# Performance work log

Measured on AMD Instinct MI355X. Metric: run time of the kernel, lower is better.

## Reference

```python
import jax, jax.numpy as jnp
import numpy as np

B, D, H, DH, DFF = 2, 1024, 16, 64, 4096
NB, NR, S = 24, 8, 512
SCALE_DEPTH = 1.4
FSQ_DIM, FSQ_LEVELS = 32, 8
EPS = 1e-5


def rmsnorm(x, w):
    var = jnp.mean(x * x, axis=-1, keepdims=True)
    return x * jax.lax.rsqrt(var + EPS) * w


def rope_cos_sin(position):
    # position: [B] int -> cos/sin [B, DH/2]
    inv = 1.0 / (10000.0 ** (jnp.arange(0, DH, 2, dtype=jnp.float32) / DH))
    ang = position.astype(jnp.float32)[:, None] * inv[None, :]
    return jnp.cos(ang), jnp.sin(ang)


def apply_rope(x, cos, sin):
    # x: [B, H, 1, DH]
    x1, x2 = jnp.split(x, 2, axis=-1)
    c = cos[:, None, None, :]
    s = sin[:, None, None, :]
    return jnp.concatenate([x1 * c - x2 * s, x1 * s + x2 * c], axis=-1)


def run_lm(hidden, cache_k, cache_v, params, cos, sin, n_layers):
    # hidden [B,1,D]; cache_k/v [L,B,H,S,DH]; params: stacked per-layer weights.
    scale = SCALE_DEPTH / np.sqrt(n_layers)  # MuP residual scale
    inv_sqrt_dh = 1.0 / np.sqrt(DH)

    def body(h, xs):
        ln1, wq, wk, wv, wo, ln2, wg, wu, wd, ck, cv = xs
        res = h
        hn = rmsnorm(h, ln1)
        q = (hn @ wq).reshape(B, 1, H, DH).transpose(0, 2, 1, 3)
        k = (hn @ wk).reshape(B, 1, H, DH).transpose(0, 2, 1, 3)
        v = (hn @ wv).reshape(B, 1, H, DH).transpose(0, 2, 1, 3)
        q = apply_rope(q, cos, sin)
        k = apply_rope(k, cos, sin)
        nk = jnp.concatenate([ck, k], axis=2)  # [B,H,S+1,DH]
        nv = jnp.concatenate([cv, v], axis=2)
        att = jnp.einsum('bhqd,bhkd->bhqk', q, nk) * inv_sqrt_dh
        p = jax.nn.softmax(att, axis=-1)
        o = jnp.einsum('bhqk,bhkd->bhqd', p, nv).transpose(0, 2, 1, 3).reshape(B, 1, D) @ wo
        h = res + o * scale
        res = h
        hn = rmsnorm(h, ln2)
        mlp = (jax.nn.silu(hn @ wg) * (hn @ wu)) @ wd
        h = res + mlp * scale
        return h, (nk, nv)

    ln1, wq, wk, wv, wo, ln2, wg, wu, wd = params
    hidden, (nk, nv) = jax.lax.scan(
        body, hidden, (ln1, wq, wk, wv, wo, ln2, wg, wu, wd, cache_k, cache_v))
    return hidden, nk, nv


def fsq(x, w_in, w_out):
    # finite scalar quantization with straight-through rounding
    z = jnp.tanh(x @ w_in)
    half = (FSQ_LEVELS - 1) / 2.0
    zq = jnp.round(z * half) / half
    zq = z + jax.lax.stop_gradient(zq - z)
    return zq @ w_out


def _forward(position, embed, base_k, base_v, res_k, res_v,
             base_ln1, base_ln2, base_wq, base_wk, base_wv, base_wo,
             base_wg, base_wu, base_wd, base_norm,
             res_ln1, res_ln2, res_wq, res_wk, res_wv, res_wo,
             res_wg, res_wu, res_wd, res_norm,
             fsq_in, fsq_out, stop_proj_w, stop_proj_b, stop_head_w, stop_head_b):
    cos, sin = rope_cos_sin(position)
    hidden, bnk, bnv = run_lm(
        embed, base_k, base_v,
        (base_ln1, base_wq, base_wk, base_wv, base_wo, base_ln2, base_wg, base_wu, base_wd),
        cos, sin, NB)
    lm_hidden = rmsnorm(hidden, base_norm)
    lm_fsq = fsq(lm_hidden, fsq_in, fsq_out)
    stop_logit = jax.nn.silu(lm_hidden @ stop_proj_w + stop_proj_b) @ stop_head_w + stop_head_b
    res_in = lm_fsq + embed
    rh, rnk, rnv = run_lm(
        res_in, res_k, res_v,
        (res_ln1, res_wq, res_wk, res_wv, res_wo, res_ln2, res_wg, res_wu, res_wd),
        cos, sin, NR)
    rh = rmsnorm(rh, res_norm)
    return (lm_fsq, rh, stop_logit, bnk, bnv, rnk, rnv)


def setup_inputs() -> dict:
    key = jax.random.key(0)
    ks = iter(jax.random.split(key, 40))

    def p(shape, scale=0.02):
        return jax.random.normal(next(ks), shape, dtype=jnp.float32) * scale

    return {
        'embed': jax.random.normal(next(ks), (B, 1, D), jnp.float32),
        'position': jax.random.randint(next(ks), (B,), 0, S),
        'base_k': jax.random.normal(next(ks), (NB, B, H, S, DH), jnp.float32),
        'base_v': jax.random.normal(next(ks), (NB, B, H, S, DH), jnp.float32),
        'res_k': jax.random.normal(next(ks), (NR, B, H, S, DH), jnp.float32),
        'res_v': jax.random.normal(next(ks), (NR, B, H, S, DH), jnp.float32),
        'base_ln1': jnp.ones((NB, D), jnp.float32),
        'base_ln2': jnp.ones((NB, D), jnp.float32),
        'base_wq': p((NB, D, D)), 'base_wk': p((NB, D, D)),
        'base_wv': p((NB, D, D)), 'base_wo': p((NB, D, D)),
        'base_wg': p((NB, D, DFF)), 'base_wu': p((NB, D, DFF)), 'base_wd': p((NB, DFF, D)),
        'base_norm': jnp.ones((D,), jnp.float32),
        'res_ln1': jnp.ones((NR, D), jnp.float32),
        'res_ln2': jnp.ones((NR, D), jnp.float32),
        'res_wq': p((NR, D, D)), 'res_wk': p((NR, D, D)),
        'res_wv': p((NR, D, D)), 'res_wo': p((NR, D, D)),
        'res_wg': p((NR, D, DFF)), 'res_wu': p((NR, D, DFF)), 'res_wd': p((NR, DFF, D)),
        'res_norm': jnp.ones((D,), jnp.float32),
        'fsq_in': p((D, FSQ_DIM)), 'fsq_out': p((FSQ_DIM, D)),
        'stop_proj_w': p((D, D)), 'stop_proj_b': jnp.zeros((D,), jnp.float32),
        'stop_head_w': p((D, 1)), 'stop_head_b': jnp.zeros((1,), jnp.float32),
    }


def reference(embed, position, base_k, base_v, res_k, res_v,
              base_ln1, base_ln2, base_wq, base_wk, base_wv, base_wo,
              base_wg, base_wu, base_wd, base_norm,
              res_ln1, res_ln2, res_wq, res_wk, res_wv, res_wo,
              res_wg, res_wu, res_wd, res_norm,
              fsq_in, fsq_out, stop_proj_w, stop_proj_b, stop_head_w, stop_head_b):
    return _forward(position, embed, base_k, base_v, res_k, res_v,
                    base_ln1, base_ln2, base_wq, base_wk, base_wv, base_wo,
                    base_wg, base_wu, base_wd, base_norm,
                    res_ln1, res_ln2, res_wq, res_wk, res_wv, res_wo,
                    res_wg, res_wu, res_wd, res_norm,
                    fsq_in, fsq_out, stop_proj_w, stop_proj_b, stop_head_w, stop_head_b)
```

## Files before the change

### kernel.cpp

```cpp
#include <hip/hip_runtime.h>
#include <cmath>

#define D 1024
#define DFF 4096
#define NHEADS 16
#define DH 64
#define S_CACHE 512
#define SP1 513
#define NB_L 24
#define NR_L 8
#define NCH 16

typedef float v4f __attribute__((ext_vector_type(4)));

#define WS_H      0
#define WS_H2     2048
#define WS_QKV    4096
#define WS_ATTN   102400
#define WS_OPROJ  137216
#define WS_GU     169984
#define WS_DOWN   301056
#define WS_SPROJ  333824

__device__ __forceinline__ float silu_f(float x){ return x/(1.f+expf(-x)); }

__device__ __forceinline__ void prologue_norm(
    const float* __restrict__ hbase,
    const float* __restrict__ part, int nks, float scale,
    const float* __restrict__ lnw,
    float (*hn)[D], float* __restrict__ hout)
{
  __shared__ float redw[4];
  const int t = threadIdx.x;
  const int b = t >> 7;
  const int i0 = (t & 127) * 8;
  const float4* hb4 = (const float4*)(hbase + b * D + i0);
  const float4 h0 = hb4[0], h1 = hb4[1];
  float acc[8] = {h0.x, h0.y, h0.z, h0.w, h1.x, h1.y, h1.z, h1.w};
  if (part != nullptr) {
    float s[8] = {0,0,0,0,0,0,0,0};
    for (int ks = 0; ks < nks; ++ks) {
      const float4* p4 = (const float4*)(part + (size_t)(ks * 2 + b) * D + i0);
      const float4 a = p4[0], c = p4[1];
      s[0]+=a.x; s[1]+=a.y; s[2]+=a.z; s[3]+=a.w;
      s[4]+=c.x; s[5]+=c.y; s[6]+=c.z; s[7]+=c.w;
    }
#pragma unroll
    for (int u = 0; u < 8; ++u) acc[u] += scale * s[u];
  }
  float ssq = 0.f;
#pragma unroll
  for (int u = 0; u < 8; ++u) ssq += acc[u] * acc[u];
#pragma unroll
  for (int off = 32; off; off >>= 1) ssq += __shfl_xor(ssq, off);
  if ((t & 63) == 0) redw[t >> 6] = ssq;
  __syncthreads();
  const float r = rsqrtf((redw[b * 2] + redw[b * 2 + 1]) * (1.f / D) + 1e-5f);
#pragma unroll
  for (int u = 0; u < 8; ++u) hn[b][i0 + u] = acc[u] * r * lnw[i0 + u];
  if (hout != nullptr && blockIdx.x == 0 && blockIdx.y == 0) {
    float4* o4 = (float4*)(hout + b * D + i0);
    o4[0] = make_float4(acc[0], acc[1], acc[2], acc[3]);
    o4[1] = make_float4(acc[4], acc[5], acc[6], acc[7]);
  }
  __syncthreads();
}

__global__ __launch_bounds__(256) void k_qkv(
    const float* __restrict__ hbase, const float* __restrict__ down_part,
    float* __restrict__ hout, const float* __restrict__ ln1,
    const float* __restrict__ wq, const float* __restrict__ wk,
    const float* __restrict__ wv,
    float* __restrict__ qkv_part, float scale, int has_prev)
{
  __shared__ float hn[2][D];
  __shared__ float redq[16][2][64];
  __shared__ float redkv[8][2][128];
  const int t = threadIdx.x;
  const int bid = blockIdx.x;
  if (bid < 256) {
    const int ks = bid >> 4, jt = bid & 15;
    const int jo4 = (t & 15) * 4;
    const int kp = t >> 4;
    const int ib = ks * 64 + kp * 4;
    float4 wbuf[4];
#pragma unroll
    for (int r = 0; r < 4; ++r)
      wbuf[r] = *(const float4*)(wq + (size_t)(ib + r) * D + jt * 64 + jo4);
    prologue_norm(hbase, has_prev ? down_part : nullptr, 16, scale, ln1, hn, hout);
    float a00=0,a01=0,a02=0,a03=0, a10=0,a11=0,a12=0,a13=0;
#pragma unroll
    for (int r = 0; r < 4; ++r) {
      const float x0 = hn[0][ib + r], x1 = hn[1][ib + r];
      a00 += wbuf[r].x*x0; a01 += wbuf[r].y*x0; a02 += wbuf[r].z*x0; a03 += wbuf[r].w*x0;
      a10 += wbuf[r].x*x1; a11 += wbuf[r].y*x1; a12 += wbuf[r].z*x1; a13 += wbuf[r].w*x1;
    }
    redq[kp][0][jo4+0]=a00; redq[kp][0][jo4+1]=a01; redq[kp][0][jo4+2]=a02; redq[kp][0][jo4+3]=a03;
    redq[kp][1][jo4+0]=a10; redq[kp][1][jo4+1]=a11; redq[kp][1][jo4+2]=a12; redq[kp][1][jo4+3]=a13;
    __syncthreads();
    if (t < 128) {
      const int b = t >> 6, jo = t & 63;
      float s = 0.f;
#pragma unroll
      for (int k2 = 0; k2 < 16; ++k2) s += redq[k2][b][jo];
      qkv_part[(size_t)((ks * 3 + 0) * 2 + b) * D + jt * 64 + jo] = s;
    }
  } else {
    const int kv = bid - 256;
    const int mat = (kv >= 128) ? 2 : 1;
    const int r2 = kv & 127;
    const int ks = r2 >> 3, jt = r2 & 7;
    const int jo4 = (t & 31) * 4;
    const int kp = t >> 5;
    const int ib = ks * 64 + kp * 8;
    const float* W = (mat == 2) ? wv : wk;
    float4 wbuf[8];
#pragma unroll
    for (int r = 0; r < 8; ++r)
      wbuf[r] = *(const float4*)(W + (size_t)(ib + r) * D + jt * 128 + jo4);
    prologue_norm(hbase, has_prev ? down_part : nullptr, 16, scale, ln1, hn, nullptr);
    float a00=0,a01=0,a02=0,a03=0, a10=0,a11=0,a12=0,a13=0;
#pragma unroll
    for (int r = 0; r < 8; ++r) {
      const float x0 = hn[0][ib + r], x1 = hn[1][ib + r];
      a00 += wbuf[r].x*x0; a01 += wbuf[r].y*x0; a02 += wbuf[r].z*x0; a03 += wbuf[r].w*x0;
      a10 += wbuf[r].x*x1; a11 += wbuf[r].y*x1; a12 += wbuf[r].z*x1; a13 += wbuf[r].w*x1;
    }
    redkv[kp][0][jo4+0]=a00; redkv[kp][0][jo4+1]=a01; redkv[kp][0][jo4+2]=a02; redkv[kp][0][jo4+3]=a03;
    redkv[kp][1][jo4+0]=a10; redkv[kp][1][jo4+1]=a11; redkv[kp][1][jo4+2]=a12; redkv[kp][1][jo4+3]=a13;
    __syncthreads();
    {
      const int b = t >> 7, jo = t & 127;
      float s = 0.f;
#pragma unroll
      for (int k2 = 0; k2 < 8; ++k2) s += redkv[k2][b][jo];
      qkv_part[(size_t)((ks * 3 + mat) * 2 + b) * D + jt * 128 + jo] = s;
    }
  }
}

__global__ __launch_bounds__(256) void k_attn(
    const float* __restrict__ qkv_part, const int* __restrict__ position,
    const float* __restrict__ k_in, const float* __restrict__ v_in,
    float* __restrict__ k_out, float* __restrict__ v_out,
    float* __restrict__ attn_part)
{
  const int t = threadIdx.x;
  const int chunk = blockIdx.x;
  const int bh = blockIdx.y;
  const int b = bh >> 4, h = bh & 15;
  const bool hasNew = (chunk == 15);
  __shared__ float q[64], kn[64], vn[64];
  __shared__ float sc[33];
  __shared__ float red8[8][32];
  __shared__ float pvred[16][64];
  __shared__ float msl[3];
  const size_t row_in  = (size_t)bh * S_CACHE;
  const size_t row_out = (size_t)bh * SP1;
  const int pbase = (bh * NCH + chunk) * 68;

  {
    const v4f* ksrc = (const v4f*)(k_in + (row_in + chunk * 32) * 64);
    const v4f* vsrc = (const v4f*)(v_in + (row_in + chunk * 32) * 64);
    v4f* kdst = (v4f*)(k_out + (row_out + chunk * 32) * 64);
    v4f* vdst = (v4f*)(v_out + (row_out + chunk * 32) * 64);
    const v4f kc0 = ksrc[t], kc1 = ksrc[t + 256];
    const v4f vc0 = vsrc[t], vc1 = vsrc[t + 256];
    __builtin_nontemporal_store(kc0, &kdst[t]);
    __builtin_nontemporal_store(kc1, &kdst[t + 256]);
    __builtin_nontemporal_store(vc0, &vdst[t]);
    __builtin_nontemporal_store(vc1, &vdst[t + 256]);
  }
  if (t < 64) {
    float s = 0.f;
#pragma unroll
    for (int ks = 0; ks < 16; ++ks)
      s += qkv_part[(size_t)(ks * 6 + b) * D + h * 64 + t];
    q[t] = s;
  } else if (hasNew && t < 128) {
    const int u = t - 64;
    float s = 0.f;
#pragma unroll
    for (int ks = 0; ks < 16; ++ks)
      s += qkv_part[(size_t)(ks * 6 + 2 + b) * D + h * 64 + u];
    kn[u] = s;
  } else if (hasNew && t < 192) {
    const int u = t - 128;
    float s = 0.f;
#pragma unroll
    for (int ks = 0; ks < 16; ++ks)
      s += qkv_part[(size_t)(ks * 6 + 4 + b) * D + h * 64 + u];
    vn[u] = s;
  }
  __syncthreads();
  {
    const float pos = (float)position[b];
    if (t < 32) {
      const float inv = expf(-(float)t * 0.28782313662425575f);
      const float ang = pos * inv;
      const float c = cosf(ang), sn = sinf(ang);
      const float x1 = q[t], x2 = q[t + 32];
      q[t]      = (x1 * c - x2 * sn) * 0.125f;
      q[t + 32] = (x1 * sn + x2 * c) * 0.125f;
    } else if (hasNew && t < 64) {
      const int u = t - 32;
      const float inv = expf(-(float)u * 0.28782313662425575f);
      const float ang = pos * inv;
      const float c = cosf(ang), sn = sinf(ang);
      const float x1 = kn[u], x2 = kn[u + 32];
      kn[u]      = x1 * c - x2 * sn;
      kn[u + 32] = x1 * sn + x2 * c;
    }
  }
  __syncthreads();
  if (hasNew && t < 64) {
    k_out[(row_out + S_CACHE) * 64 + t] = kn[t];
    v_out[(row_out + S_CACHE) * 64 + t] = vn[t];
    float dp = q[t] * kn[t];
#pragma unroll
    for (int off = 32; off; off >>= 1) dp += __shfl_xor(dp, off);
    if (t == 0) msl[0] = dp;
  }
  {
    const int key = t & 31, kp = t >> 5;
    const float* krow = k_in + (row_in + chunk * 32 + key) * 64 + kp * 8;
    const float4 k0 = *(const float4*)krow;
    const float4 k1 = *(const float4*)(krow + 4);
    const int d = kp * 8;
    float dp = k0.x*q[d] + k0.y*q[d+1] + k0.z*q[d+2] + k0.w*q[d+3]
             + k1.x*q[d+4] + k1.y*q[d+5] + k1.z*q[d+6] + k1.w*q[d+7];
    red8[kp][key] = dp;
  }
  __syncthreads();
  if (t < 32) {
    float score = 0.f;
#pragma unroll
    for (int k2 = 0; k2 < 8; ++k2) score += red8[k2][t];
    float m = score;
#pragma unroll
    for (int off = 16; off; off >>= 1) m = fmaxf(m, __shfl_xor(m, off));
    const float nsc = hasNew ? msl[0] : -1e30f;
    m = fmaxf(m, nsc);
    const float p = expf(score - m);
    float l = p;
#pragma unroll
    for (int off = 16; off; off >>= 1) l += __shfl_xor(l, off);
    sc[t] = p;
    if (t == 0) {
      const float pn = hasNew ? expf(nsc - m) : 0.f;
      sc[32] = pn; msl[1] = m; msl[2] = l + pn;
    }
  }
  __syncthreads();
  {
    const int d4 = (t & 15) * 4, sp = t >> 4;
    float ax = 0.f, ay = 0.f, az = 0.f, aw = 0.f;
#pragma unroll
    for (int r = 0; r < 2; ++r) {
      const int sl = sp * 2 + r;
      const float4 vv = *(const float4*)(v_in + (row_in + chunk * 32 + sl) * 64 + d4);
      const float p2 = sc[sl];
      ax += vv.x * p2; ay += vv.y * p2; az += vv.z * p2; aw += vv.w * p2;
    }
    pvred[sp][d4+0]=ax; pvred[sp][d4+1]=ay; pvred[sp][d4+2]=az; pvred[sp][d4+3]=aw;
  }
  __syncthreads();
  if (t < 64) {
    float a = 0.f;
#pragma unroll
    for (int s2 = 0; s2 < 16; ++s2) a += pvred[s2][t];
    if (hasNew) a += sc[32] * vn[t];
    attn_part[pbase + 2 + t] = a;
    if (t == 0) { attn_part[pbase + 0] = msl[1]; attn_part[pbase + 1] = msl[2]; }
  }
}

__global__ __launch_bounds__(256) void k_oproj(
    const float* __restrict__ attn_part, const float* __restrict__ wo,
    float* __restrict__ oproj_part)
{
  __shared__ float o[2][64];
  __shared__ float cw[2][NCH];
  __shared__ float redg[32][2][32];
  __shared__ float redqq[4][2][32];
  const int t = threadIdx.x;
  const int ks = blockIdx.x;
  const int cg = blockIdx.y;
  const int ibeg = ks * 64;
  const int jbase = cg * 32;
  const int jo4 = (t & 7) * 4;
  const int kp = t >> 3;
  float4 wbuf[2];
#pragma unroll
  for (int r = 0; r < 2; ++r)
    wbuf[r] = *(const float4*)(wo + (size_t)(ibeg + kp * 2 + r) * D + jbase + jo4);
  if (t < 2) {
    const int bb = t;
    const int base = ((bb * 16 + ks) * NCH) * 68;
    float mg = -1e30f;
    for (int c = 0; c < NCH; ++c) mg = fmaxf(mg, attn_part[base + c * 68]);
    float lg = 0.f;
    float wloc[NCH];
    for (int c = 0; c < NCH; ++c) {
      const float w = expf(attn_part[base + c * 68] - mg);
      wloc[c] = w;
      lg += attn_part[base + c * 68 + 1] * w;
    }
    const float invl = 1.f / lg;
    for (int c = 0; c < NCH; ++c) cw[bb][c] = wloc[c] * invl;
  }
  __syncthreads();
  if (t < 128) {
    const int bb = t >> 6, d = t & 63;
    float s = 0.f;
#pragma unroll
    for (int c = 0; c < NCH; ++c)
      s += attn_part[((bb * 16 + ks) * NCH + c) * 68 + 2 + d] * cw[bb][c];
    o[bb][d] = s;
  }
  __syncthreads();
  float a00=0,a01=0,a02=0,a03=0, a10=0,a11=0,a12=0,a13=0;
#pragma unroll
  for (int r = 0; r < 2; ++r) {
    const int ir = kp * 2 + r;
    const float x0 = o[0][ir], x1 = o[1][ir];
    a00 += wbuf[r].x*x0; a01 += wbuf[r].y*x0; a02 += wbuf[r].z*x0; a03 += wbuf[r].w*x0;
    a10 += wbuf[r].x*x1; a11 += wbuf[r].y*x1; a12 += wbuf[r].z*x1; a13 += wbuf[r].w*x1;
  }
  redg[kp][0][jo4+0]=a00; redg[kp][0][jo4+1]=a01; redg[kp][0][jo4+2]=a02; redg[kp][0][jo4+3]=a03;
  redg[kp][1][jo4+0]=a10; redg[kp][1][jo4+1]=a11; redg[kp][1][jo4+2]=a12; redg[kp][1][jo4+3]=a13;
  __syncthreads();
  {
    const int qq = t >> 6, rest = t & 63;
    const int b2 = rest >> 5, jo = rest & 31;
    float s = 0.f;
#pragma unroll
    for (int k2 = 0; k2 < 8; ++k2) s += redg[qq * 8 + k2][b2][jo];
    redqq[qq][b2][jo] = s;
  }
  __syncthreads();
  if (t < 64) {
    const int b2 = t >> 5, jo = t & 31;
    const float s = redqq[0][b2][jo] + redqq[1][b2][jo] + redqq[2][b2][jo] + redqq[3][b2][jo];
    oproj_part[(size_t)(ks * 2 + b2) * D + jbase + jo] = s;
  }
}

__global__ __launch_bounds__(256) void k_gateup(
    const float* __restrict__ hbase, const float* __restrict__ oproj_part,
    float* __restrict__ h2_out, const float* __restrict__ ln2,
    const float* __restrict__ wg, const float* __restrict__ wu,
    float* __restrict__ gu_part, float scale)
{
  __shared__ float hn[2][D];
  __shared__ float redg[16][4][64];
  const int t = threadIdx.x;
  const int ks = blockIdx.x;
  const int cg = blockIdx.y;
  const int jbase = cg * 64;
  const int jo4 = (t & 15) * 4;
  const int kp = t >> 4;
  const int ib = ks * 128 + kp * 8;
  float4 wgb[8];
#pragma unroll
  for (int r = 0; r < 8; ++r)
    wgb[r] = *(const float4*)(wg + (size_t)(ib + r) * DFF + jbase + jo4);
  prologue_norm(hbase, oproj_part, 16, scale, ln2, hn, h2_out);
  float g00=0,g01=0,g02=0,g03=0, g10=0,g11=0,g12=0,g13=0;
  float u00=0,u01=0,u02=0,u03=0, u10=0,u11=0,u12=0,u13=0;
#pragma unroll
  for (int r = 0; r < 8; ++r) {
    const float x0 = hn[0][ib + r], x1 = hn[1][ib + r];
    g00 += wgb[r].x*x0; g01 += wgb[r].y*x0; g02 += wgb[r].z*x0; g03 += wgb[r].w*x0;
    g10 += wgb[r].x*x1; g11 += wgb[r].y*x1; g12 += wgb[r].z*x1; g13 += wgb[r].w*x1;
  }
#pragma unroll
  for (int r = 0; r < 8; ++r) {
    const float4 c = *(const float4*)(wu + (size_t)(ib + r) * DFF + jbase + jo4);
    const float x0 = hn[0][ib + r], x1 = hn[1][ib + r];
    u00 += c.x*x0; u01 += c.y*x0; u02 += c.z*x0; u03 += c.w*x0;
    u10 += c.x*x1; u11 += c.y*x1; u12 += c.z*x1; u13 += c.w*x1;
  }
  redg[kp][0][jo4+0]=g00; redg[kp][0][jo4+1]=g01; redg[kp][0][jo4+2]=g02; redg[kp][0][jo4+3]=g03;
  redg[kp][1][jo4+0]=g10; redg[kp][1][jo4+1]=g11; redg[kp][1][jo4+2]=g12; redg[kp][1][jo4+3]=g13;
  redg[kp][2][jo4+0]=u00; redg[kp][2][jo4+1]=u01; redg[kp][2][jo4+2]=u02; redg[kp][2][jo4+3]=u03;
  redg[kp][3][jo4+0]=u10; redg[kp][3][jo4+1]=u11; redg[kp][3][jo4+2]=u12; redg[kp][3][jo4+3]=u13;
  __syncthreads();
  {
    const int sel = t >> 6;
    const int jo = t & 63;
    float s = 0.f;
#pragma unroll
    for (int k2 = 0; k2 < 16; ++k2) s += redg[k2][sel][jo];
    const int gm = sel >> 1, b = sel & 1;
    gu_part[(size_t)(ks * 4 + gm * 2 + b) * DFF + jbase + jo] = s;
  }
}

__global__ __launch_bounds__(256) void k_down(
    const float* __restrict__ gu_part, const float* __restrict__ wd,
    float* __restrict__ down_part)
{
  __shared__ float act[2][256];
  __shared__ float redg[32][2][32];
  __shared__ float redqq[4][2][32];
  const int t = threadIdx.x;
  const int ks = blockIdx.x;
  const int cg = blockIdx.y;
  const int ibeg = ks * 256;
  const int jbase = cg * 32;
  const int jo4 = (t & 7) * 4;
  const int kp = t >> 3;
  float4 wbuf[8];
#pragma unroll
  for (int r = 0; r < 8; ++r)
    wbuf[r] = *(const float4*)(wd + (size_t)(ibeg + kp * 8 + r) * D + jbase + jo4);
#pragma unroll
  for (int u = 0; u < 2; ++u) {
    const int e = u * 256 + t;
    const int b = e >> 8, ir = e & 255;
    const int i = ibeg + ir;
    float g = 0.f, uu = 0.f;
#pragma unroll
    for (int k = 0; k < 8; ++k) {
      g  += gu_part[(size_t)(k * 4 + b) * DFF + i];
      uu += gu_part[(size_t)(k * 4 + 2 + b) * DFF + i];
    }
    act[b][ir] = silu_f(g) * uu;
  }
  __syncthreads();
  float a00=0,a01=0,a02=0,a03=0, a10=0,a11=0,a12=0,a13=0;
#pragma unroll
  for (int r = 0; r < 8; ++r) {
    const int lr = kp * 8 + r;
    const float x0 = act[0][lr], x1 = act[1][lr];
    a00 += wbuf[r].x*x0; a01 += wbuf[r].y*x0; a02 += wbuf[r].z*x0; a03 += wbuf[r].w*x0;
    a10 += wbuf[r].x*x1; a11 += wbuf[r].y*x1; a12 += wbuf[r].z*x1; a13 += wbuf[r].w*x1;
  }
  redg[kp][0][jo4+0]=a00; redg[kp][0][jo4+1]=a01; redg[kp][0][jo4+2]=a02; redg[kp][0][jo4+3]=a03;
  redg[kp][1][jo4+0]=a10; redg[kp][1][jo4+1]=a11; redg[kp][1][jo4+2]=a12; redg[kp][1][jo4+3]=a13;
  __syncthreads();
  {
    const int qq = t >> 6, rest = t & 63;
    const int b2 = rest >> 5, jo = rest & 31;
    float s = 0.f;
#pragma unroll
    for (int k2 = 0; k2 < 8; ++k2) s += redg[qq * 8 + k2][b2][jo];
    redqq[qq][b2][jo] = s;
  }
  __syncthreads();
  if (t < 64) {
    const int b2 = t >> 5, jo = t & 31;
    const float s = redqq[0][b2][jo] + redqq[1][b2][jo] + redqq[2][b2][jo] + redqq[3][b2][jo];
    down_part[(size_t)(ks * 2 + b2) * D + jbase + jo] = s;
  }
}

__global__ __launch_bounds__(256) void k_heads(
    const float* __restrict__ hbase, const float* __restrict__ down_part,
    const float* __restrict__ normw, const float* __restrict__ wsp,
    float* __restrict__ sproj_part,
    const float* __restrict__ fsq_in, const float* __restrict__ fsq_out,
    const float* __restrict__ embed,
    float* __restrict__ out_fsq, float* __restrict__ h_res, float scale)
{
  __shared__ float hn[2][D];
  const int t = threadIdx.x;
  const int bid = blockIdx.x;
  if (bid < 128) {
    __shared__ float redg[16][2][64];
    const int ks = bid >> 4, cg = bid & 15;
    const int jbase = cg * 64;
    const int jo4 = (t & 15) * 4;
    const int kp = t >> 4;
    const int ib = ks * 128 + kp * 8;
    float4 wbuf[8];
#pragma unroll
    for (int r = 0; r < 8; ++r)
      wbuf[r] = *(const float4*)(wsp + (size_t)(ib + r) * D + jbase + jo4);
    prologue_norm(hbase, down_part, 16, scale, normw, hn, nullptr);
    float a00=0,a01=0,a02=0,a03=0, a10=0,a11=0,a12=0,a13=0;
#pragma unroll
    for (int r = 0; r < 8; ++r) {
      const float x0 = hn[0][ib + r], x1 = hn[1][ib + r];
      a00 += wbuf[r].x*x0; a01 += wbuf[r].y*x0; a02 += wbuf[r].z*x0; a03 += wbuf[r].w*x0;
      a10 += wbuf[r].x*x1; a11 += wbuf[r].y*x1; a12 += wbuf[r].z*x1; a13 += wbuf[r].w*x1;
    }
    redg[kp][0][jo4+0]=a00; redg[kp][0][jo4+1]=a01; redg[kp][0][jo4+2]=a02; redg[kp][0][jo4+3]=a03;
    redg[kp][1][jo4+0]=a10; redg[kp][1][jo4+1]=a11; redg[kp][1][jo4+2]=a12; redg[kp][1][jo4+3]=a13;
    __syncthreads();
    if (t < 128) {
      const int b = t >> 6, jo = t & 63;
      float s = 0.f;
#pragma unroll
      for (int k2 = 0; k2 < 16; ++k2) s += redg[k2][b][jo];
      sproj_part[(size_t)(ks * 2 + b) * D + jbase + jo] = s;
    }
  } else {
    __shared__ float zred[4][2][32];
    __shared__ float zq[2][32];
    prologue_norm(hbase, down_part, 16, scale, normw, hn, nullptr);
    {
      const int c = t & 31, b = (t >> 5) & 1, kp = t >> 6;
      float s = 0.f;
      for (int i = kp * 256; i < kp * 256 + 256; ++i) s += hn[b][i] * fsq_in[i * 32 + c];
      zred[kp][b][c] = s;
    }
    __syncthreads();
    if (t < 64) {
      const int b = t >> 5, c = t & 31;
      float z = zred[0][b][c] + zred[1][b][c] + zred[2][b][c] + zred[3][b][c];
      z = tanhf(z);
      zq[b][c] = rintf(z * 3.5f) / 3.5f;
    }
    __syncthreads();
    if (t < 128) {
      const int b = t >> 6, jo = t & 63;
      const int j = (bid - 128) * 64 + jo;
      float s = 0.f;
#pragma unroll
      for (int c = 0; c < 32; ++c) s += zq[b][c] * fsq_out[c * D + j];
      out_fsq[b * D + j] = s;
      h_res[b * D + j] = s + embed[b * D + j];
    }
  }
}

__global__ __launch_bounds__(256) void k_stophead(
    const float* __restrict__ sproj_part, const float* __restrict__ bvec,
    const float* __restrict__ hw, const float* __restrict__ hb,
    float* __restrict__ out_stop)
{
  const int t = threadIdx.x;
  float acc0 = 0.f, acc1 = 0.f;
  for (int j = t; j < D; j += 256) {
    float v0 = bvec[j], v1 = bvec[j];
#pragma unroll
    for (int ks = 0; ks < 8; ++ks) {
      v0 += sproj_part[(ks * 2 + 0) * D + j];
      v1 += sproj_part[(ks * 2 + 1) * D + j];
    }
    acc0 += silu_f(v0) * hw[j];
    acc1 += silu_f(v1) * hw[j];
  }
  __shared__ float red[256];
  red[t] = acc0;
  __syncthreads();
  for (int s = 128; s > 0; s >>= 1) { if (t < s) red[t] += red[t + s]; __syncthreads(); }
  if (t == 0) out_stop[0] = red[0] + hb[0];
  __syncthreads();
  red[t] = acc1;
  __syncthreads();
  for (int s = 128; s > 0; s >>= 1) { if (t < s) red[t] += red[t + s]; __syncthreads(); }
  if (t == 0) out_stop[1] = red[0] + hb[0];
}

__global__ __launch_bounds__(256) void k_final(
    const float* __restrict__ hbase, const float* __restrict__ down_part,
    const float* __restrict__ normw, float* __restrict__ out_rh, float scale)
{
  __shared__ float hn[2][D];
  prologue_norm(hbase, down_part, 16, scale, normw, hn, nullptr);
  const int t = threadIdx.x;
  const int b = t >> 7;
  const int i0 = (t & 127) * 8;
#pragma unroll
  for (int u = 0; u < 8; ++u) out_rh[b * D + i0 + u] = hn[b][i0 + u];
}

extern "C" void kernel_launch(void* const* d_in, const int* in_sizes, int n_in,
                              void* d_out, int out_size, void* d_ws, size_t ws_size,
                              hipStream_t stream) {
  const float* embed      = (const float*)d_in[0];
  const int*   position   = (const int*)d_in[1];
  const float* base_k     = (const float*)d_in[2];
  const float* base_v     = (const float*)d_in[3];
  const float* res_k      = (const float*)d_in[4];
  const float* res_v      = (const float*)d_in[5];
  const float* base_ln1   = (const float*)d_in[6];
  const float* base_ln2   = (const float*)d_in[7];
  const float* base_wq    = (const float*)d_in[8];
  const float* base_wk    = (const float*)d_in[9];
  const float* base_wv    = (const float*)d_in[10];
  const float* base_wo    = (const float*)d_in[11];
  const float* base_wg    = (const float*)d_in[12];
  const float* base_wu    = (const float*)d_in[13];
  const float* base_wd    = (const float*)d_in[14];
  const float* base_norm  = (const float*)d_in[15];
  const float* res_ln1    = (const float*)d_in[16];
  const float* res_ln2    = (const float*)d_in[17];
  const float* res_wq     = (const float*)d_in[18];
  const float* res_wk     = (const float*)d_in[19];
  const float* res_wv     = (const float*)d_in[20];
  const float* res_wo     = (const float*)d_in[21];
  const float* res_wg     = (const float*)d_in[22];
  const float* res_wu     = (const float*)d_in[23];
  const float* res_wd     = (const float*)d_in[24];
  const float* res_norm   = (const float*)d_in[25];
  const float* fsq_in     = (const float*)d_in[26];
  const float* fsq_out    = (const float*)d_in[27];
  const float* stop_proj_w = (const float*)d_in[28];
  const float* stop_proj_b = (const float*)d_in[29];
  const float* stop_head_w = (const float*)d_in[30];
  const float* stop_head_b = (const float*)d_in[31];

  float* out = (float*)d_out;
  float* ws = (float*)d_ws;
  float* W_h     = ws + WS_H;
  float* W_h2    = ws + WS_H2;
  float* W_qkv   = ws + WS_QKV;
  float* W_attn  = ws + WS_ATTN;
  float* W_oproj = ws + WS_OPROJ;
  float* W_gu    = ws + WS_GU;
  float* W_down  = ws + WS_DOWN;
  float* W_sproj = ws + WS_SPROJ;

  const size_t cacheL_in  = (size_t)2 * NHEADS * S_CACHE * DH;
  const size_t cacheL_out = (size_t)2 * NHEADS * SP1 * DH;
  float* out_fsq  = out;
  float* out_rh   = out + 2048;
  float* out_stop = out + 4096;
  float* out_bnk  = out + 4098;
  float* out_bnv  = out_bnk + (size_t)NB_L * cacheL_out;
  float* out_rnk  = out_bnv + (size_t)NB_L * cacheL_out;
  float* out_rnv  = out_rnk + (size_t)NR_L * cacheL_out;

  const float scaleB = 1.4f / sqrtf((float)NB_L);
  const float scaleR = 1.4f / sqrtf((float)NR_L);

  auto run_layer = [&](const float* hbase, float* hout,
                       const float* ln1, const float* ln2,
                       const float* wq, const float* wk, const float* wv,
                       const float* wo, const float* wg, const float* wu,
                       const float* wd,
                       const float* kin, const float* vin,
                       float* kout, float* vout,
                       float scale, int has_prev) {
    k_qkv<<<512, 256, 0, stream>>>(hbase, W_down, hout, ln1,
                                   wq, wk, wv, W_qkv, scale, has_prev);
    k_attn<<<dim3(NCH, 32), 256, 0, stream>>>(W_qkv, position, kin, vin, kout, vout, W_attn);
    k_oproj<<<dim3(16, 32), 256, 0, stream>>>(W_attn, wo, W_oproj);
    k_gateup<<<dim3(8, 64), 256, 0, stream>>>(W_h, W_oproj, W_h2, ln2, wg, wu, W_gu, scale);
    k_down<<<dim3(16, 32), 256, 0, stream>>>(W_gu, wd, W_down);
  };

  for (int l = 0; l < NB_L; ++l) {
    run_layer(l == 0 ? embed : W_h2, W_h,
              base_ln1 + (size_t)l * D, base_ln2 + (size_t)l * D,
              base_wq + (size_t)l * D * D, base_wk + (size_t)l * D * D,
              base_wv + (size_t)l * D * D, base_wo + (size_t)l * D * D,
              base_wg + (size_t)l * D * DFF, base_wu + (size_t)l * D * DFF,
              base_wd + (size_t)l * DFF * D,
              base_k + (size_t)l * cacheL_in, base_v + (size_t)l * cacheL_in,
              out_bnk + (size_t)l * cacheL_out, out_bnv + (size_t)l * cacheL_out,
              scaleB, l > 0);
  }

  k_heads<<<144, 256, 0, stream>>>(W_h2, W_down, base_norm, stop_proj_w, W_sproj,
                                   fsq_in, fsq_out, embed, out_fsq, W_h, scaleB);
  k_stophead<<<1, 256, 0, stream>>>(W_sproj, stop_proj_b, stop_head_w, stop_head_b, out_stop);

  for (int l = 0; l < NR_L; ++l) {
    run_layer(l == 0 ? W_h : W_h2, l == 0 ? nullptr : W_h,
              res_ln1 + (size_t)l * D, res_ln2 + (size_t)l * D,
              res_wq + (size_t)l * D * D, res_wk + (size_t)l * D * D,
              res_wv + (size_t)l * D * D, res_wo + (size_t)l * D * D,
              res_wg + (size_t)l * D * DFF, res_wu + (size_t)l * D * DFF,
              res_wd + (size_t)l * DFF * D,
              res_k + (size_t)l * cacheL_in, res_v + (size_t)l * cacheL_in,
              out_rnk + (size_t)l * cacheL_out, out_rnv + (size_t)l * cacheL_out,
              scaleR, l > 0);
  }

  k_final<<<1, 256, 0, stream>>>(W_h2, W_down, res_norm, out_rh, scaleR);
}
```

Before: 1.181 ms.

## Halve k-splits in oproj/down GEMVs and preload gate+up weights together

The o-projection and down-projection GEMVs switch from 16 k-splits with 32-column tiles to 8 k-splits with 16-column tiles, so each block covers two heads or 512 rows. This halves the partial-sum buffers that downstream prologue_norm calls must reduce, and the workspace offsets shrink to match. Gate-up now loads both the gate and up weight tiles into registers before the norm prologue, so all weight loads are in flight together. The costs are higher register pressure and narrower column tiles, which may weaken coalescing on weight reads (16 floats per row segment).

```diff
diff --git a/kernel.cpp b/kernel.cpp
--- a/kernel.cpp
+++ b/kernel.cpp
@@ -18,9 +18,9 @@
 #define WS_QKV    4096
 #define WS_ATTN   102400
 #define WS_OPROJ  137216
-#define WS_GU     169984
-#define WS_DOWN   301056
-#define WS_SPROJ  333824
+#define WS_GU     153600
+#define WS_DOWN   284672
+#define WS_SPROJ  301056
 
 __device__ __forceinline__ float silu_f(float x){ return x/(1.f+expf(-x)); }
 
@@ -87,7 +87,7 @@
 #pragma unroll
     for (int r = 0; r < 4; ++r)
       wbuf[r] = *(const float4*)(wq + (size_t)(ib + r) * D + jt * 64 + jo4);
-    prologue_norm(hbase, has_prev ? down_part : nullptr, 16, scale, ln1, hn, hout);
+    prologue_norm(hbase, has_prev ? down_part : nullptr, 8, scale, ln1, hn, hout);
     float a00=0,a01=0,a02=0,a03=0, a10=0,a11=0,a12=0,a13=0;
 #pragma unroll
     for (int r = 0; r < 4; ++r) {
@@ -118,7 +118,7 @@
 #pragma unroll
     for (int r = 0; r < 8; ++r)
       wbuf[r] = *(const float4*)(W + (size_t)(ib + r) * D + jt * 128 + jo4);
-    prologue_norm(hbase, has_prev ? down_part : nullptr, 16, scale, ln1, hn, nullptr);
+    prologue_norm(hbase, has_prev ? down_part : nullptr, 8, scale, ln1, hn, nullptr);
     float a00=0,a01=0,a02=0,a03=0, a10=0,a11=0,a12=0,a13=0;
 #pragma unroll
     for (int r = 0; r < 8; ++r) {
@@ -279,24 +279,25 @@
     const float* __restrict__ attn_part, const float* __restrict__ wo,
     float* __restrict__ oproj_part)
 {
-  __shared__ float o[2][64];
-  __shared__ float cw[2][NCH];
-  __shared__ float redg[32][2][32];
-  __shared__ float redqq[4][2][32];
+  __shared__ float o[2][128];
+  __shared__ float cw[4][NCH];
+  __shared__ float redg[64][2][16];
+  __shared__ float redq2[8][2][16];
   const int t = threadIdx.x;
   const int ks = blockIdx.x;
-  const int cg = blockIdx.y;
-  const int ibeg = ks * 64;
-  const int jbase = cg * 32;
-  const int jo4 = (t & 7) * 4;
-  const int kp = t >> 3;
+  const int jt = blockIdx.y;
+  const int ibeg = ks * 128;
+  const int jbase = jt * 16;
+  const int jo4 = (t & 3) * 4;
+  const int kp = t >> 2;
   float4 wbuf[2];
 #pragma unroll
   for (int r = 0; r < 2; ++r)
     wbuf[r] = *(const float4*)(wo + (size_t)(ibeg + kp * 2 + r) * D + jbase + jo4);
-  if (t < 2) {
-    const int bb = t;
-    const int base = ((bb * 16 + ks) * NCH) * 68;
+  if (t < 4) {
+    const int bb = t >> 1, hr = t & 1;
+    const int hh = ks * 2 + hr;
+    const int base = ((bb * 16 + hh) * NCH) * 68;
     float mg = -1e30f;
     for (int c = 0; c < NCH; ++c) mg = fmaxf(mg, attn_part[base + c * 68]);
     float lg = 0.f;
@@ -307,16 +308,18 @@
       lg += attn_part[base + c * 68 + 1] * w;
     }
     const float invl = 1.f / lg;
-    for (int c = 0; c < NCH; ++c) cw[bb][c] = wloc[c] * invl;
-  }
-  __syncthreads();
-  if (t < 128) {
-    const int bb = t >> 6, d = t & 63;
+    for (int c = 0; c < NCH; ++c) cw[bb * 2 + hr][c] = wloc[c] * invl;
+  }
+  __syncthreads();
+  {
+    const int bb = t >> 7, ir = t & 127;
+    const int i = ibeg + ir;
+    const int hh = i >> 6, hr = hh - ks * 2, d = i & 63;
     float s = 0.f;
 #pragma unroll
     for (int c = 0; c < NCH; ++c)
-      s += attn_part[((bb * 16 + ks) * NCH + c) * 68 + 2 + d] * cw[bb][c];
-    o[bb][d] = s;
+      s += attn_part[((bb * 16 + hh) * NCH + c) * 68 + 2 + d] * cw[bb * 2 + hr][c];
+    o[bb][ir] = s;
   }
   __syncthreads();
   float a00=0,a01=0,a02=0,a03=0, a10=0,a11=0,a12=0,a13=0;
@@ -331,17 +334,19 @@
   redg[kp][1][jo4+0]=a10; redg[kp][1][jo4+1]=a11; redg[kp][1][jo4+2]=a12; redg[kp][1][jo4+3]=a13;
   __syncthreads();
   {
-    const int qq = t >> 6, rest = t & 63;
-    const int b2 = rest >> 5, jo = rest & 31;
+    const int qq = t >> 5, rest = t & 31;
+    const int b2 = rest >> 4, jo = rest & 15;
     float s = 0.f;
 #pragma unroll
     for (int k2 = 0; k2 < 8; ++k2) s += redg[qq * 8 + k2][b2][jo];
-    redqq[qq][b2][jo] = s;
-  }
-  __syncthreads();
-  if (t < 64) {
-    const int b2 = t >> 5, jo = t & 31;
-    const float s = redqq[0][b2][jo] + redqq[1][b2][jo] + redqq[2][b2][jo] + redqq[3][b2][jo];
+    redq2[qq][b2][jo] = s;
+  }
+  __syncthreads();
+  if (t < 32) {
+    const int b2 = t >> 4, jo = t & 15;
+    float s = 0.f;
+#pragma unroll
+    for (int q2 = 0; q2 < 8; ++q2) s += redq2[q2][b2][jo];
     oproj_part[(size_t)(ks * 2 + b2) * D + jbase + jo] = s;
   }
 }
@@ -361,25 +366,23 @@
   const int jo4 = (t & 15) * 4;
   const int kp = t >> 4;
   const int ib = ks * 128 + kp * 8;
-  float4 wgb[8];
+  float4 wb[16];
 #pragma unroll
   for (int r = 0; r < 8; ++r)
-    wgb[r] = *(const float4*)(wg + (size_t)(ib + r) * DFF + jbase + jo4);
-  prologue_norm(hbase, oproj_part, 16, scale, ln2, hn, h2_out);
+    wb[r] = *(const float4*)(wg + (size_t)(ib + r) * DFF + jbase + jo4);
+#pragma unroll
+  for (int r = 0; r < 8; ++r)
+    wb[8 + r] = *(const float4*)(wu + (size_t)(ib + r) * DFF + jbase + jo4);
+  prologue_norm(hbase, oproj_part, 8, scale, ln2, hn, h2_out);
   float g00=0,g01=0,g02=0,g03=0, g10=0,g11=0,g12=0,g13=0;
   float u00=0,u01=0,u02=0,u03=0, u10=0,u11=0,u12=0,u13=0;
 #pragma unroll
   for (int r = 0; r < 8; ++r) {
     const float x0 = hn[0][ib + r], x1 = hn[1][ib + r];
-    g00 += wgb[r].x*x0; g01 += wgb[r].y*x0; g02 += wgb[r].z*x0; g03 += wgb[r].w*x0;
-    g10 += wgb[r].x*x1; g11 += wgb[r].y*x1; g12 += wgb[r].z*x1; g13 += wgb[r].w*x1;
-  }
-#pragma unroll
-  for (int r = 0; r < 8; ++r) {
-    const float4 c = *(const float4*)(wu + (size_t)(ib + r) * DFF + jbase + jo4);
-    const float x0 = hn[0][ib + r], x1 = hn[1][ib + r];
-    u00 += c.x*x0; u01 += c.y*x0; u02 += c.z*x0; u03 += c.w*x0;
-    u10 += c.x*x1; u11 += c.y*x1; u12 += c.z*x1; u13 += c.w*x1;
+    g00 += wb[r].x*x0; g01 += wb[r].y*x0; g02 += wb[r].z*x0; g03 += wb[r].w*x0;
+    g10 += wb[r].x*x1; g11 += wb[r].y*x1; g12 += wb[r].z*x1; g13 += wb[r].w*x1;
+    u00 += wb[8+r].x*x0; u01 += wb[8+r].y*x0; u02 += wb[8+r].z*x0; u03 += wb[8+r].w*x0;
+    u10 += wb[8+r].x*x1; u11 += wb[8+r].y*x1; u12 += wb[8+r].z*x1; u13 += wb[8+r].w*x1;
   }
   redg[kp][0][jo4+0]=g00; redg[kp][0][jo4+1]=g01; redg[kp][0][jo4+2]=g02; redg[kp][0][jo4+3]=g03;
   redg[kp][1][jo4+0]=g10; redg[kp][1][jo4+1]=g11; redg[kp][1][jo4+2]=g12; redg[kp][1][jo4+3]=g13;
@@ -401,24 +404,24 @@
     const float* __restrict__ gu_part, const float* __restrict__ wd,
     float* __restrict__ down_part)
 {
-  __shared__ float act[2][256];
-  __shared__ float redg[32][2][32];
-  __shared__ float redqq[4][2][32];
+  __shared__ float act[2][512];
+  __shared__ float redg[64][2][16];
+  __shared__ float redq2[8][2][16];
   const int t = threadIdx.x;
   const int ks = blockIdx.x;
-  const int cg = blockIdx.y;
-  const int ibeg = ks * 256;
-  const int jbase = cg * 32;
-  const int jo4 = (t & 7) * 4;
-  const int kp = t >> 3;
+  const int jt = blockIdx.y;
+  const int ibeg = ks * 512;
+  const int jbase = jt * 16;
+  const int jo4 = (t & 3) * 4;
+  const int kp = t >> 2;
   float4 wbuf[8];
 #pragma unroll
   for (int r = 0; r < 8; ++r)
     wbuf[r] = *(const float4*)(wd + (size_t)(ibeg + kp * 8 + r) * D + jbase + jo4);
 #pragma unroll
-  for (int u = 0; u < 2; ++u) {
+  for (int u = 0; u < 4; ++u) {
     const int e = u * 256 + t;
-    const int b = e >> 8, ir = e & 255;
+    const int b = e >> 9, ir = e & 511;
     const int i = ibeg + ir;
     float g = 0.f, uu = 0.f;
 #pragma unroll
@@ -441,17 +444,19 @@
   redg[kp][1][jo4+0]=a10; redg[kp][1][jo4+1]=a11; redg[kp][1][jo4+2]=a12; redg[kp][1][jo4+3]=a13;
   __syncthreads();
   {
-    const int qq = t >> 6, rest = t & 63;
-    const int b2 = rest >> 5, jo = rest & 31;
+    const int qq = t >> 5, rest = t & 31;
+    const int b2 = rest >> 4, jo = rest & 15;
     float s = 0.f;
 #pragma unroll
     for (int k2 = 0; k2 < 8; ++k2) s += redg[qq * 8 + k2][b2][jo];
-    redqq[qq][b2][jo] = s;
-  }
-  __syncthreads();
-  if (t < 64) {
-    const int b2 = t >> 5, jo = t & 31;
-    const float s = redqq[0][b2][jo] + redqq[1][b2][jo] + redqq[2][b2][jo] + redqq[3][b2][jo];
+    redq2[qq][b2][jo] = s;
+  }
+  __syncthreads();
+  if (t < 32) {
+    const int b2 = t >> 4, jo = t & 15;
+    float s = 0.f;
+#pragma unroll
+    for (int q2 = 0; q2 < 8; ++q2) s += redq2[q2][b2][jo];
     down_part[(size_t)(ks * 2 + b2) * D + jbase + jo] = s;
   }
 }
@@ -478,7 +483,7 @@
 #pragma unroll
     for (int r = 0; r < 8; ++r)
       wbuf[r] = *(const float4*)(wsp + (size_t)(ib + r) * D + jbase + jo4);
-    prologue_norm(hbase, down_part, 16, scale, normw, hn, nullptr);
+    prologue_norm(hbase, down_part, 8, scale, normw, hn, nullptr);
     float a00=0,a01=0,a02=0,a03=0, a10=0,a11=0,a12=0,a13=0;
 #pragma unroll
     for (int r = 0; r < 8; ++r) {
@@ -499,7 +504,7 @@
   } else {
     __shared__ float zred[4][2][32];
     __shared__ float zq[2][32];
-    prologue_norm(hbase, down_part, 16, scale, normw, hn, nullptr);
+    prologue_norm(hbase, down_part, 8, scale, normw, hn, nullptr);
     {
       const int c = t & 31, b = (t >> 5) & 1, kp = t >> 6;
       float s = 0.f;
@@ -560,7 +565,7 @@
     const float* __restrict__ normw, float* __restrict__ out_rh, float scale)
 {
   __shared__ float hn[2][D];
-  prologue_norm(hbase, down_part, 16, scale, normw, hn, nullptr);
+  prologue_norm(hbase, down_part, 8, scale, normw, hn, nullptr);
   const int t = threadIdx.x;
   const int b = t >> 7;
   const int i0 = (t & 127) * 8;
@@ -639,9 +644,9 @@
     k_qkv<<<512, 256, 0, stream>>>(hbase, W_down, hout, ln1,
                                    wq, wk, wv, W_qkv, scale, has_prev);
     k_attn<<<dim3(NCH, 32), 256, 0, stream>>>(W_qkv, position, kin, vin, kout, vout, W_attn);
-    k_oproj<<<dim3(16, 32), 256, 0, stream>>>(W_attn, wo, W_oproj);
+    k_oproj<<<dim3(8, 64), 256, 0, stream>>>(W_attn, wo, W_oproj);
     k_gateup<<<dim3(8, 64), 256, 0, stream>>>(W_h, W_oproj, W_h2, ln2, wg, wu, W_gu, scale);
-    k_down<<<dim3(16, 32), 256, 0, stream>>>(W_gu, wd, W_down);
+    k_down<<<dim3(8, 64), 256, 0, stream>>>(W_gu, wd, W_down);
   };
 
   for (int l = 0; l < NB_L; ++l) {
```

Result: faster. 1.152 ms (-2.5%).
